# Optimization experiments

Measured on AMD Instinct MI355X. Metric: run time of the kernel, lower is better.

The kernel has to match this reference:

```python
import jax, jax.numpy as jnp
import numpy as np

TEMP = 0.07
BASE_TEMP = 0.07
BANK = 8192
B = 512      # samples per view; features has 2*B rows
D = 128      # feature dim
N_CLASSES = 100


def _l2norm(x, axis=-1):
    return x / jnp.linalg.norm(x, axis=axis, keepdims=True)


def setup_inputs() -> dict:
    key = jax.random.key(0)
    k1, k2, k3, k4, k5 = jax.random.split(key, 5)
    # SupCon features are L2-normalized embeddings; two views stacked: [2B, 1, D]
    features = _l2norm(jax.random.normal(k1, (2 * B, 1, D), jnp.float32))
    label = jax.random.randint(k2, (B,), 0, N_CLASSES)
    # memory banks stored as [D, bank_size] (lightly MemoryBankModule layout)
    bank1 = _l2norm(jax.random.normal(k3, (D, BANK), jnp.float32), axis=0)
    bank2 = _l2norm(jax.random.normal(k4, (D, BANK), jnp.float32), axis=0)
    bank_labels = jax.random.randint(k5, (BANK,), 0, N_CLASSES)
    return {"features": features, "label": label, "bank1": bank1,
            "bank2": bank2, "bank_labels": bank_labels}


def _branch_loss(cf, pos_mask, neg_mask):
    # cf: [N, D] anchor==contrast features
    logits = jnp.matmul(cf, cf.T) / TEMP                       # [N, N]
    logits = logits - jax.lax.stop_gradient(logits.max(axis=1, keepdims=True))
    # denominator: sum of exp(logits) over NEGATIVES only (square(mask-1) mask)
    denom = jnp.log((jnp.exp(logits) * neg_mask).sum(axis=1, keepdims=True))
    log_prob = logits - denom                                  # [N, N]
    mean_log_prob_pos = (pos_mask * log_prob).sum(axis=1) / pos_mask.sum(axis=1)
    return -(TEMP / BASE_TEMP) * mean_log_prob_pos             # [N]


def reference(features, label, bank1, bank2, bank_labels):
    d = features.shape[-1]
    fr = features.reshape(-1, d)                # [2B, D]
    nb = fr.shape[0] // 2
    f1, f2 = fr[:nb], fr[nb:]                   # [B, D] each

    labels_all = jnp.concatenate([bank_labels.reshape(-1, 1),
                                  label.reshape(-1, 1)], axis=0)   # [N, 1]
    same = (labels_all == labels_all.T)                            # [N, N]
    mask = same.astype(fr.dtype)
    n = mask.shape[0]
    self_mask = 1.0 - jnp.eye(n, dtype=fr.dtype)
    pos_mask = mask * self_mask                 # positives excluding self
    neg_mask = jnp.square(mask - 1.0)           # 1 where labels differ

    cf1 = jnp.concatenate([bank2.T, f1], axis=0)   # [N, D]
    cf2 = jnp.concatenate([bank1.T, f2], axis=0)   # [N, D]

    class_loss = (_branch_loss(cf1, pos_mask, neg_mask)
                  + _branch_loss(cf2, pos_mask, neg_mask)) / 2.0
    loss = class_loss.mean()
    return (loss, loss, loss)
```

## Files before the change

kernel.cpp:

```cpp
#include <hip/hip_runtime.h>
#include <math.h>

#define NTOT 8704
#define BANKN 8192
#define NB 512
#define DIM 128
#define INVT (1.0f / 0.07f)
#define C2L 20.6099131801f
#define NCHUNK 17
#define TPC 8
#define BN 64

using short8 = __attribute__((ext_vector_type(8))) short;
using ushort8 = __attribute__((ext_vector_type(8))) unsigned short;
using f32x4 = __attribute__((ext_vector_type(4))) float;

static __device__ __forceinline__ ushort f2bf(float f) {
  union { float f; unsigned u; } v;
  v.f = f;
  unsigned r = v.u + 0x7fffu + ((v.u >> 16) & 1u);
  return (ushort)(r >> 16);
}

static __device__ __forceinline__ float fast_exp2(float x) {
#if __has_builtin(__builtin_amdgcn_exp2f)
  return __builtin_amdgcn_exp2f(x);
#else
  return exp2f(x);
#endif
}

__global__ __launch_bounds__(1024) void prep_kernel(
    const int* __restrict__ bank_labels, const int* __restrict__ label,
    int* __restrict__ inv, int* __restrict__ lo, int* __restrict__ hi,
    float* __restrict__ zp) {
  __shared__ int h[101];
  __shared__ int st[101];
  __shared__ int cur[100];
  const int tid = threadIdx.x;
  for (int i = tid; i < NTOT; i += 1024)
    reinterpret_cast<float4*>(zp)[i] = make_float4(0.f, 0.f, 0.f, 0.f);
  if (tid < 101) h[tid] = 0;
  __syncthreads();
  for (int i = tid; i < NTOT; i += 1024) {
    const int v = (i < BANKN) ? bank_labels[i] : label[i - BANKN];
    atomicAdd(&h[v], 1);
  }
  __syncthreads();
  if (tid == 0) {
    int s = 0;
    for (int c = 0; c < 100; ++c) { st[c] = s; s += h[c]; }
    st[100] = s;
  }
  __syncthreads();
  if (tid < 100) cur[tid] = st[tid];
  __syncthreads();
  for (int i = tid; i < NTOT; i += 1024) {
    const int v = (i < BANKN) ? bank_labels[i] : label[i - BANKN];
    const int p = atomicAdd(&cur[v], 1);
    inv[i] = p;
    lo[p] = st[v];
    hi[p] = st[v + 1];
  }
}

__global__ void pack_kernel(const float* __restrict__ features,
                            const float* __restrict__ bank1,
                            const float* __restrict__ bank2,
                            const int* __restrict__ inv,
                            ushort* __restrict__ cf1b,
                            ushort* __restrict__ cf2b) {
  const int branch = blockIdx.z;
  ushort* __restrict__ dst = branch ? cf2b : cf1b;
  const int tx = threadIdx.x, ty = threadIdx.y;
  const int bx = blockIdx.x, by = blockIdx.y;
  if (bx < 256) {
    const float* __restrict__ src = branch ? bank1 : bank2;
    __shared__ float tile[32][33];
    const int col = bx * 32 + tx;
#pragma unroll
    for (int s = 0; s < 32; s += 8)
      tile[ty + s][tx] = src[(size_t)(by * 32 + ty + s) * BANKN + col];
    __syncthreads();
    const int k = by * 32 + tx;
#pragma unroll
    for (int s = 0; s < 32; s += 8) {
      const int p = inv[bx * 32 + ty + s];
      dst[(size_t)p * DIM + k] = f2bf(tile[tx][ty + s]);
    }
  } else {
    const int j = (bx - 256) * 32 + ty;
#pragma unroll
    for (int s = 0; s < 32; s += 8) {
      const int jr = (bx - 256) * 32 + ty + s;
      const int k = by * 32 + tx;
      const float v = features[(size_t)(branch * NB + jr) * DIM + k];
      const int p = inv[BANKN + jr];
      dst[(size_t)p * DIM + k] = f2bf(v);
    }
    (void)j;
  }
}

__global__ __launch_bounds__(256) void supcon_mfma_kernel(
    const ushort* __restrict__ cf1b, const ushort* __restrict__ cf2b,
    const int* __restrict__ lo, const int* __restrict__ hi,
    float* __restrict__ zp) {
  const int rb = blockIdx.x;
  const int chunk = blockIdx.y;
  const int branch = blockIdx.z;
  const ushort* __restrict__ cf = branch ? cf2b : cf1b;

  const int tid = threadIdx.x;
  const int wid = tid >> 6, lane = tid & 63;
  const int l15 = lane & 15, l4 = lane >> 4;
  const int rowW = rb * 128 + wid * 32;

  __shared__ ushort Bt[2][BN * DIM];

  short8 a[2][4];
#pragma unroll
  for (int rt = 0; rt < 2; ++rt) {
    const int r = rowW + rt * 16 + l15;
#pragma unroll
    for (int ks = 0; ks < 4; ++ks)
      a[rt][ks] = *reinterpret_cast<const short8*>(cf + (size_t)r * DIM + ks * 32 + l4 * 8);
  }
  int rlo[2][4], rhi[2][4];
#pragma unroll
  for (int rt = 0; rt < 2; ++rt)
#pragma unroll
    for (int rg = 0; rg < 4; ++rg) {
      const int rr = rowW + rt * 16 + l4 * 4 + rg;
      rlo[rt][rg] = lo[rr];
      rhi[rt][rg] = hi[rr];
    }
  const int u_lo = lo[rowW];
  const int u_hi = hi[rowW + 31];
  const int lo_last = lo[rowW + 31];
  const int hi_first = hi[rowW];

  float Zr[2][4] = {{0.f, 0.f, 0.f, 0.f}, {0.f, 0.f, 0.f, 0.f}};
  float Pr[2][4] = {{0.f, 0.f, 0.f, 0.f}, {0.f, 0.f, 0.f, 0.f}};

  auto STAGE = [&](int t, int buf) {
    const int col0 = (chunk * TPC + t) * BN;
#pragma unroll
    for (int it = 0; it < 4; ++it) {
      const int o = it * 256 + tid;
      const int row = o >> 4, cc = o & 15;
      const ushort* src =
          cf + (size_t)(col0 + row) * DIM + ((cc ^ (row & 7)) * 8);
      ushort* dst = &Bt[buf][(it * 256 + wid * 64) * 8];
      __builtin_amdgcn_global_load_lds(
          (const __attribute__((address_space(1))) void*)src,
          (__attribute__((address_space(3))) void*)dst, 16, 0, 0);
    }
  };

  STAGE(0, 0);
  asm volatile("s_waitcnt vmcnt(0)" ::: "memory");
  __syncthreads();

  int cur = 0;
  for (int t = 0; t < TPC; ++t) {
    if (t + 1 < TPC) STAGE(t + 1, cur ^ 1);

    const int col0 = (chunk * TPC + t) * BN;

    f32x4 acc[2][4];
#pragma unroll
    for (int rt = 0; rt < 2; ++rt)
#pragma unroll
      for (int ct = 0; ct < 4; ++ct) acc[rt][ct] = (f32x4){0.f, 0.f, 0.f, 0.f};

#pragma unroll
    for (int ks = 0; ks < 4; ++ks) {
      short8 b[4];
#pragma unroll
      for (int ct = 0; ct < 4; ++ct) {
        const int r = ct * 16 + l15;
        const int swz = (ks * 4 + l4) ^ (r & 7);
        b[ct] = *reinterpret_cast<const short8*>(&Bt[cur][r * DIM + swz * 8]);
      }
#pragma unroll
      for (int rt = 0; rt < 2; ++rt)
#pragma unroll
        for (int ct = 0; ct < 4; ++ct)
          acc[rt][ct] = __builtin_amdgcn_mfma_f32_16x16x32_bf16(
              a[rt][ks], b[ct], acc[rt][ct], 0, 0, 0);
    }

    if (col0 + BN <= u_lo || col0 >= u_hi) {
#pragma unroll
      for (int ct = 0; ct < 4; ++ct)
#pragma unroll
        for (int rt = 0; rt < 2; ++rt)
#pragma unroll
          for (int rg = 0; rg < 4; ++rg)
            Zr[rt][rg] += fast_exp2(fmaf(acc[rt][ct][rg], C2L, -C2L));
    } else if (col0 >= lo_last && col0 + BN <= hi_first) {
#pragma unroll
      for (int ct = 0; ct < 4; ++ct)
#pragma unroll
        for (int rt = 0; rt < 2; ++rt)
#pragma unroll
          for (int rg = 0; rg < 4; ++rg) Pr[rt][rg] += acc[rt][ct][rg];
    } else {
#pragma unroll
      for (int ct = 0; ct < 4; ++ct) {
        const int c = col0 + ct * 16 + l15;
#pragma unroll
        for (int rt = 0; rt < 2; ++rt)
#pragma unroll
          for (int rg = 0; rg < 4; ++rg) {
            const float v = acc[rt][ct][rg];
            const float e = fast_exp2(fmaf(v, C2L, -C2L));
            const bool s = (c >= rlo[rt][rg]) && (c < rhi[rt][rg]);
            Zr[rt][rg] += s ? 0.0f : e;
            Pr[rt][rg] += s ? v : 0.0f;
          }
      }
    }

    asm volatile("s_waitcnt vmcnt(0)" ::: "memory");
    __syncthreads();
    cur ^= 1;
  }

  float* Zrow = zp;
  float* Prow = zp + 2 * NTOT;
#pragma unroll
  for (int rt = 0; rt < 2; ++rt)
#pragma unroll
    for (int rg = 0; rg < 4; ++rg) {
      float z = Zr[rt][rg], p = Pr[rt][rg];
#pragma unroll
      for (int off = 1; off < 16; off <<= 1) {
        z += __shfl_xor(z, off);
        p += __shfl_xor(p, off);
      }
      if (l15 == 0) {
        const int row = rowW + rt * 16 + l4 * 4 + rg;
        atomicAdd(&Zrow[branch * NTOT + row], z);
        atomicAdd(&Prow[branch * NTOT + row], p);
      }
    }
}

__global__ __launch_bounds__(1024) void loss_kernel(const float* __restrict__ zp,
                                                    const int* __restrict__ lo,
                                                    const int* __restrict__ hi,
                                                    float* __restrict__ out) {
  const int tid = threadIdx.x;
  const float* Zrow = zp;
  const float* Prow = zp + 2 * NTOT;
  float local = 0.f;
  for (int idx = tid; idx < 2 * NTOT; idx += 1024) {
    const int row = (idx >= NTOT) ? idx - NTOT : idx;
    const float z = Zrow[idx];
    const float p = Prow[idx];
    const float C = (float)(hi[row] - lo[row] - 1);
    const float denom = INVT + logf(z);
    local += -((INVT * (p - 1.0f)) / C - denom);
  }
  __shared__ float s[1024];
  s[tid] = local;
  __syncthreads();
  for (int st = 512; st > 0; st >>= 1) {
    if (tid < st) s[tid] += s[tid + st];
    __syncthreads();
  }
  if (tid == 0) {
    const float v = s[0] / (2.0f * NTOT);
    out[0] = v; out[1] = v; out[2] = v;
  }
}

extern "C" void kernel_launch(void* const* d_in, const int* in_sizes, int n_in,
                              void* d_out, int out_size, void* d_ws,
                              size_t ws_size, hipStream_t stream) {
  const float* features = (const float*)d_in[0];
  const int* label = (const int*)d_in[1];
  const float* bank1 = (const float*)d_in[2];
  const float* bank2 = (const float*)d_in[3];
  const int* bank_labels = (const int*)d_in[4];
  float* out = (float*)d_out;

  char* ws = (char*)d_ws;
  ushort* cf1b = (ushort*)(ws);
  ushort* cf2b = (ushort*)(ws + 2228224);
  int* inv = (int*)(ws + 4456448);
  int* lo = (int*)(ws + 4491264);
  int* hi = (int*)(ws + 4526080);
  float* zp = (float*)(ws + 4560896);

  prep_kernel<<<dim3(1), dim3(1024), 0, stream>>>(bank_labels, label, inv, lo,
                                                  hi, zp);
  pack_kernel<<<dim3(272, DIM / 32, 2), dim3(32, 8), 0, stream>>>(
      features, bank1, bank2, inv, cf1b, cf2b);
  supcon_mfma_kernel<<<dim3(NTOT / 128, NCHUNK, 2), dim3(256), 0, stream>>>(
      cf1b, cf2b, lo, hi, zp);
  loss_kernel<<<dim3(1), dim3(1024), 0, stream>>>(zp, lo, hi, out);
}
```

Before: 154.0 us.

## Triple-buffer MFMA tile loads, parallelize prep histogram/scan, move zeroing to pack

The main kernel goes from double to triple buffering of B tiles, with two loads in flight and a single barrier per iteration, so global-to-LDS loads overlap more with MFMA work. The LDS swizzle widens from 8 to 16 chunks to reduce bank conflicts. The single-block prep kernel now keeps per-wave histograms and uses a parallel prefix scan instead of a serial one, cutting its atomic contention and serial time. Zeroing the accumulators moves from prep into the parallel pack kernel. The extra buffer raises LDS use per block, and the single barrier with vmcnt(4) depends on each thread issuing exactly four loads per stage.

```diff
diff --git a/kernel.cpp b/kernel.cpp
--- a/kernel.cpp
+++ b/kernel.cpp
@@ -32,32 +32,54 @@
 
 __global__ __launch_bounds__(1024) void prep_kernel(
     const int* __restrict__ bank_labels, const int* __restrict__ label,
-    int* __restrict__ inv, int* __restrict__ lo, int* __restrict__ hi,
-    float* __restrict__ zp) {
-  __shared__ int h[101];
+    int* __restrict__ inv, int* __restrict__ lo, int* __restrict__ hi) {
+  __shared__ int h[16][100];
   __shared__ int st[101];
-  __shared__ int cur[100];
+  __shared__ int sc[128];
   const int tid = threadIdx.x;
-  for (int i = tid; i < NTOT; i += 1024)
-    reinterpret_cast<float4*>(zp)[i] = make_float4(0.f, 0.f, 0.f, 0.f);
-  if (tid < 101) h[tid] = 0;
+  const int w = tid >> 6;
+  for (int i = tid; i < 1600; i += 1024) (&h[0][0])[i] = 0;
   __syncthreads();
   for (int i = tid; i < NTOT; i += 1024) {
     const int v = (i < BANKN) ? bank_labels[i] : label[i - BANKN];
-    atomicAdd(&h[v], 1);
-  }
-  __syncthreads();
-  if (tid == 0) {
-    int s = 0;
-    for (int c = 0; c < 100; ++c) { st[c] = s; s += h[c]; }
-    st[100] = s;
-  }
-  __syncthreads();
-  if (tid < 100) cur[tid] = st[tid];
+    atomicAdd(&h[w][v], 1);
+  }
+  __syncthreads();
+  int tot = 0;
+  if (tid < 128) {
+    if (tid < 100) {
+#pragma unroll
+      for (int w2 = 0; w2 < 16; ++w2) tot += h[w2][tid];
+    }
+    sc[tid] = tot;
+  }
+  __syncthreads();
+#pragma unroll
+  for (int off = 1; off < 128; off <<= 1) {
+    int add = 0;
+    if (tid < 128 && tid >= off) add = sc[tid - off];
+    __syncthreads();
+    if (tid < 128) sc[tid] += add;
+    __syncthreads();
+  }
+  if (tid < 100) {
+    st[tid] = sc[tid] - tot;
+    if (tid == 99) st[100] = sc[99];
+  }
+  __syncthreads();
+  if (tid < 100) {
+    int base = st[tid];
+#pragma unroll
+    for (int w2 = 0; w2 < 16; ++w2) {
+      const int t = h[w2][tid];
+      h[w2][tid] = base;
+      base += t;
+    }
+  }
   __syncthreads();
   for (int i = tid; i < NTOT; i += 1024) {
     const int v = (i < BANKN) ? bank_labels[i] : label[i - BANKN];
-    const int p = atomicAdd(&cur[v], 1);
+    const int p = atomicAdd(&h[w][v], 1);
     inv[i] = p;
     lo[p] = st[v];
     hi[p] = st[v + 1];
@@ -69,11 +91,19 @@
                             const float* __restrict__ bank2,
                             const int* __restrict__ inv,
                             ushort* __restrict__ cf1b,
-                            ushort* __restrict__ cf2b) {
+                            ushort* __restrict__ cf2b,
+                            float* __restrict__ zp) {
   const int branch = blockIdx.z;
   ushort* __restrict__ dst = branch ? cf2b : cf1b;
   const int tx = threadIdx.x, ty = threadIdx.y;
   const int bx = blockIdx.x, by = blockIdx.y;
+  const int tid = ty * 32 + tx;
+  {
+    const int bid = (blockIdx.z * gridDim.y + blockIdx.y) * gridDim.x + bx;
+    const int gid = bid * 256 + tid;
+    if (gid < NTOT)
+      reinterpret_cast<float4*>(zp)[gid] = make_float4(0.f, 0.f, 0.f, 0.f);
+  }
   if (bx < 256) {
     const float* __restrict__ src = branch ? bank1 : bank2;
     __shared__ float tile[32][33];
@@ -89,7 +119,6 @@
       dst[(size_t)p * DIM + k] = f2bf(tile[tx][ty + s]);
     }
   } else {
-    const int j = (bx - 256) * 32 + ty;
 #pragma unroll
     for (int s = 0; s < 32; s += 8) {
       const int jr = (bx - 256) * 32 + ty + s;
@@ -98,7 +127,6 @@
       const int p = inv[BANKN + jr];
       dst[(size_t)p * DIM + k] = f2bf(v);
     }
-    (void)j;
   }
 }
 
@@ -116,7 +144,7 @@
   const int l15 = lane & 15, l4 = lane >> 4;
   const int rowW = rb * 128 + wid * 32;
 
-  __shared__ ushort Bt[2][BN * DIM];
+  __shared__ ushort Bt[3][BN * DIM];
 
   short8 a[2][4];
 #pragma unroll
@@ -140,8 +168,8 @@
   const int lo_last = lo[rowW + 31];
   const int hi_first = hi[rowW];
 
-  float Zr[2][4] = {{0.f, 0.f, 0.f, 0.f}, {0.f, 0.f, 0.f, 0.f}};
-  float Pr[2][4] = {{0.f, 0.f, 0.f, 0.f}, {0.f, 0.f, 0.f, 0.f}};
+  float Zr[2][4] = {};
+  float Pr[2][4] = {};
 
   auto STAGE = [&](int t, int buf) {
     const int col0 = (chunk * TPC + t) * BN;
@@ -150,7 +178,7 @@
       const int o = it * 256 + tid;
       const int row = o >> 4, cc = o & 15;
       const ushort* src =
-          cf + (size_t)(col0 + row) * DIM + ((cc ^ (row & 7)) * 8);
+          cf + (size_t)(col0 + row) * DIM + ((cc ^ (row & 15)) * 8);
       ushort* dst = &Bt[buf][(it * 256 + wid * 64) * 8];
       __builtin_amdgcn_global_load_lds(
           (const __attribute__((address_space(1))) void*)src,
@@ -159,14 +187,18 @@
   };
 
   STAGE(0, 0);
-  asm volatile("s_waitcnt vmcnt(0)" ::: "memory");
-  __syncthreads();
-
-  int cur = 0;
+  STAGE(1, 1);
+
   for (int t = 0; t < TPC; ++t) {
-    if (t + 1 < TPC) STAGE(t + 1, cur ^ 1);
+    if (t + 1 < TPC)
+      asm volatile("s_waitcnt vmcnt(4)" ::: "memory");
+    else
+      asm volatile("s_waitcnt vmcnt(0)" ::: "memory");
+    __builtin_amdgcn_s_barrier();
+    if (t + 2 < TPC) STAGE(t + 2, (t + 2) % 3);
 
     const int col0 = (chunk * TPC + t) * BN;
+    const ushort* __restrict__ B = &Bt[t % 3][0];
 
     f32x4 acc[2][4];
 #pragma unroll
@@ -180,8 +212,8 @@
 #pragma unroll
       for (int ct = 0; ct < 4; ++ct) {
         const int r = ct * 16 + l15;
-        const int swz = (ks * 4 + l4) ^ (r & 7);
-        b[ct] = *reinterpret_cast<const short8*>(&Bt[cur][r * DIM + swz * 8]);
+        const int swz = (ks * 4 + l4) ^ (r & 15);
+        b[ct] = *reinterpret_cast<const short8*>(&B[r * DIM + swz * 8]);
       }
 #pragma unroll
       for (int rt = 0; rt < 2; ++rt)
@@ -222,10 +254,6 @@
           }
       }
     }
-
-    asm volatile("s_waitcnt vmcnt(0)" ::: "memory");
-    __syncthreads();
-    cur ^= 1;
   }
 
   float* Zrow = zp;
@@ -296,9 +324,9 @@
   float* zp = (float*)(ws + 4560896);
 
   prep_kernel<<<dim3(1), dim3(1024), 0, stream>>>(bank_labels, label, inv, lo,
-                                                  hi, zp);
+                                                  hi);
   pack_kernel<<<dim3(272, DIM / 32, 2), dim3(32, 8), 0, stream>>>(
-      features, bank1, bank2, inv, cf1b, cf2b);
+      features, bank1, bank2, inv, cf1b, cf2b, zp);
   supcon_mfma_kernel<<<dim3(NTOT / 128, NCHUNK, 2), dim3(256), 0, stream>>>(
       cf1b, cf2b, lo, hi, zp);
   loss_kernel<<<dim3(1), dim3(1024), 0, stream>>>(zp, lo, hi, out);
```

Result: no change. 151.2 us (-1.8%).
